# Kernel tuning notes

Hardware: AMD Instinct MI355X
Metric: run time of the kernel (lower is better)

Reference implementation:

```python
import jax, jax.numpy as jnp
import numpy as np

B, S, D, H = 2, 2048, 1024, 16
DK = D // H


def setup_inputs() -> dict:
    key = jax.random.key(0)
    ks = jax.random.split(key, 12)
    scale = 1.0 / np.sqrt(D)
    inp = {
        "q": jax.random.normal(ks[0], (B, S, D), dtype=jnp.float32),
        "k": jax.random.normal(ks[1], (B, S, D), dtype=jnp.float32),
        "v": jax.random.normal(ks[2], (B, S, D), dtype=jnp.float32),
        "mask": jax.random.randint(ks[3], (B, 1, 1, S), 0, 2, dtype=jnp.int32),
        "Wq": jax.random.normal(ks[4], (D, D), dtype=jnp.float32) * scale,
        "bq": jnp.zeros((D,), dtype=jnp.float32),
        "Wk": jax.random.normal(ks[5], (D, D), dtype=jnp.float32) * scale,
        "bk": jnp.zeros((D,), dtype=jnp.float32),
        "Wv": jax.random.normal(ks[6], (D, D), dtype=jnp.float32) * scale,
        "bv": jnp.zeros((D,), dtype=jnp.float32),
        "Wo": jax.random.normal(ks[7], (D, D), dtype=jnp.float32) * scale,
        "bo": jnp.zeros((D,), dtype=jnp.float32),
    }
    return inp


def reference(q, k, v, mask, Wq, bq, Wk, bk, Wv, bv, Wo, bo):
    # Linear projections (torch nn.Linear: x @ W.T + b)
    query = q @ Wq.T + bq                      # [B,S,D]
    key = k @ Wk.T + bk
    value = v @ Wv.T + bv
    # split heads -> [B,H,S,DK]
    def split(x):
        return x.reshape(B, S, H, DK).transpose(0, 2, 1, 3)
    qh, kh, vh = split(query), split(key), split(value)
    # scaled dot-product attention with additive mask
    scores = jnp.einsum("bhqd,bhkd->bhqk", qh, kh) / jnp.sqrt(jnp.float32(DK))
    scores = jnp.where(mask == 0, jnp.float32(-1e9), scores)
    attn = jax.nn.softmax(scores, axis=-1)     # [B,H,S,S]
    out = jnp.einsum("bhqk,bhkd->bhqd", attn, vh)
    out = out.transpose(0, 2, 1, 3).reshape(B, S, D)
    return out @ Wo.T + bo
```

## Files before the change

kernel.cpp:

```cpp
#include <hip/hip_runtime.h>


constexpr int BB = 2;
constexpr int SS = 2048;
constexpr int DD = 1024;
constexpr int HH = 16;
constexpr int DKK = 64;

typedef float f32x4 __attribute__((ext_vector_type(4)));
typedef __bf16 bf16x8 __attribute__((ext_vector_type(8)));
typedef short s16x8 __attribute__((ext_vector_type(8)));
typedef short s16x4 __attribute__((ext_vector_type(4)));

#define DEV static __device__ __forceinline__

DEV f32x4 mfma16(s16x8 a, s16x8 b, f32x4 c) {
  return __builtin_amdgcn_mfma_f32_16x16x32_bf16(
      __builtin_bit_cast(bf16x8, a), __builtin_bit_cast(bf16x8, b), c, 0, 0, 0);
}

DEV void split1(float x, short& h, short& l) {
  unsigned u = __float_as_uint(x);
  h = (short)(u >> 16);
  float hf = __uint_as_float(u & 0xffff0000u);
  l = (short)(__float_as_uint(x - hf) >> 16);
}
DEV short f2bf_rne(float x) {
  unsigned u = __float_as_uint(x);
  return (short)((u + 0x7fffu + ((u >> 16) & 1u)) >> 16);
}
DEV s16x8 load8s(const short* p) { return *(const s16x8*)p; }

DEV void gld_lds16(const short* g, short* l) {
  __builtin_amdgcn_global_load_lds(
      (const __attribute__((address_space(1))) void*)g,
      (__attribute__((address_space(3))) void*)l, 16, 0, 0);
}

__global__ __launch_bounds__(256) void split_pair(const float* __restrict__ X,
                                                  short* __restrict__ H,
                                                  short* __restrict__ L) {
  int i = (blockIdx.x * 256 + threadIdx.x) * 4;
  float4 x = *(const float4*)(X + i);
  float xs[4] = {x.x, x.y, x.z, x.w};
  s16x4 h4, l4;
#pragma unroll
  for (int e = 0; e < 4; ++e) {
    short h, l;
    split1(xs[e], h, l);
    h4[e] = h;
    l4[e] = l;
  }
  *(s16x4*)(H + i) = h4;
  *(s16x4*)(L + i) = l4;
}

__global__ __launch_bounds__(256) void cast_rne(const float* __restrict__ X,
                                                short* __restrict__ Y) {
  int i = (blockIdx.x * 256 + threadIdx.x) * 4;
  float4 x = *(const float4*)(X + i);
  float xs[4] = {x.x, x.y, x.z, x.w};
  s16x4 y4;
#pragma unroll
  for (int e = 0; e < 4; ++e) y4[e] = f2bf_rne(xs[e]);
  *(s16x4*)(Y + i) = y4;
}

template <int SPLIT, int EPI>
__global__ __launch_bounds__(256) void gemm_tile(
    const short* __restrict__ Agh, const short* __restrict__ Agl,
    const short* __restrict__ Wgh, const short* __restrict__ Wgl,
    const float* __restrict__ bias, void* __restrict__ O1, void* __restrict__ O2) {
  __shared__ short lds[2][12288];

  const int tid = threadIdx.x;
  const int lane = tid & 63, wv = tid >> 6;
  const int lo16 = lane & 15, quad = lane >> 4;
  const int m0 = (blockIdx.x & 31) * 128;
  const int n0 = (blockIdx.x >> 5) * 64;

  f32x4 acc[2][4];
#pragma unroll
  for (int mt = 0; mt < 2; ++mt)
#pragma unroll
    for (int nt = 0; nt < 4; ++nt) acc[mt][nt] = f32x4{0.f, 0.f, 0.f, 0.f};

  const int rw = tid >> 2, qw = tid & 3;
  const int ra0 = tid >> 2, ra1 = (tid + 256) >> 2;

  auto stage = [&](int k0, int buf) {
    short* sAh = lds[buf];
    short* sAl = lds[buf] + 4096;
    short* sWh = lds[buf] + 8192;
    short* sWl = lds[buf] + 10240;
    gld_lds16(Wgh + (size_t)(n0 + rw) * DD + k0 + qw * 8, sWh + tid * 8);
    if constexpr (SPLIT)
      gld_lds16(Wgl + (size_t)(n0 + rw) * DD + k0 + qw * 8, sWl + tid * 8);
    gld_lds16(Agh + (size_t)(m0 + ra0) * DD + k0 + qw * 8, sAh + tid * 8);
    gld_lds16(Agh + (size_t)(m0 + ra1) * DD + k0 + qw * 8, sAh + (tid + 256) * 8);
    if constexpr (SPLIT) {
      gld_lds16(Agl + (size_t)(m0 + ra0) * DD + k0 + qw * 8, sAl + tid * 8);
      gld_lds16(Agl + (size_t)(m0 + ra1) * DD + k0 + qw * 8, sAl + (tid + 256) * 8);
    }
  };

  stage(0, 0);

  for (int kk = 0; kk < DD / 32; ++kk) {
    __syncthreads();
    if (kk + 1 < DD / 32) stage((kk + 1) * 32, (kk + 1) & 1);

    const short* sAh = lds[kk & 1];
    const short* sAl = lds[kk & 1] + 4096;
    const short* sWh = lds[kk & 1] + 8192;
    const short* sWl = lds[kk & 1] + 10240;

    s16x8 ah[2], al[2], wh[4], wl[4];
#pragma unroll
    for (int mt = 0; mt < 2; ++mt) {
      const int r = wv * 32 + mt * 16 + lo16;
      ah[mt] = *(const s16x8*)&sAh[r * 32 + quad * 8];
      if constexpr (SPLIT) al[mt] = *(const s16x8*)&sAl[r * 32 + quad * 8];
    }
#pragma unroll
    for (int nt = 0; nt < 4; ++nt) {
      const int r = nt * 16 + lo16;
      wh[nt] = *(const s16x8*)&sWh[r * 32 + quad * 8];
      if constexpr (SPLIT) wl[nt] = *(const s16x8*)&sWl[r * 32 + quad * 8];
    }
#pragma unroll
    for (int mt = 0; mt < 2; ++mt)
#pragma unroll
      for (int nt = 0; nt < 4; ++nt) {
        acc[mt][nt] = mfma16(ah[mt], wh[nt], acc[mt][nt]);
        if constexpr (SPLIT) {
          acc[mt][nt] = mfma16(ah[mt], wl[nt], acc[mt][nt]);
          acc[mt][nt] = mfma16(al[mt], wh[nt], acc[mt][nt]);
        }
      }
  }

#pragma unroll
  for (int mt = 0; mt < 2; ++mt)
#pragma unroll
    for (int nt = 0; nt < 4; ++nt) {
      const int n = n0 + nt * 16 + lo16;
      const float bv = bias[n];
#pragma unroll
      for (int r = 0; r < 4; ++r) {
        const int m = m0 + wv * 32 + mt * 16 + quad * 4 + r;
        const float val = acc[mt][nt][r] + bv;
        const int b = m >> 11, s = m & 2047;
        const int h = n >> 6, dk = n & 63;
        if constexpr (EPI == 0) {
          size_t idx = ((size_t)(b * HH + h) * SS + s) * DKK + dk;
          short hh, ll;
          split1(val, hh, ll);
          ((short*)O1)[idx] = hh;
          ((short*)O2)[idx] = ll;
        } else if constexpr (EPI == 1) {
          size_t idx = ((size_t)(b * HH + h) * DKK + dk) * SS + s;
          ((short*)O1)[idx] = f2bf_rne(val);
        } else {
          ((float*)O1)[(size_t)m * DD + n] = val;
        }
      }
    }
}

constexpr int PAD = 68;
constexpr int NKB = SS / 64;

__global__ __launch_bounds__(256, 2) void mha_attn(
    const short* __restrict__ Qh, const short* __restrict__ Ql,
    const short* __restrict__ Kh, const short* __restrict__ Kl,
    const short* __restrict__ Vt, const int* __restrict__ mask,
    short* __restrict__ Ah, short* __restrict__ Al) {
  __shared__ short sKh[64 * PAD];
  __shared__ short sKl[64 * PAD];
  __shared__ short sV[64 * PAD];
  __shared__ short sP[4][32 * PAD];

  const int tid = threadIdx.x;
  const int lane = tid & 63, wv = tid >> 6;
  const int lo16 = lane & 15, quad = lane >> 4;
  const int bid = blockIdx.x;
  const int head = (bid & 7) * 4 + ((bid >> 3) & 3);
  const int qblk = bid >> 5;
  const int q0 = qblk * 128 + wv * 32;
  const int b = head >> 4;

  const size_t hbase = (size_t)head * SS;

  s16x8 qh[2][2], ql[2][2];
#pragma unroll
  for (int rt = 0; rt < 2; ++rt) {
    size_t qb = (hbase + q0 + rt * 16 + lo16) * DKK + quad * 8;
#pragma unroll
    for (int c = 0; c < 2; ++c) {
      qh[rt][c] = load8s(Qh + qb + c * 32);
      ql[rt][c] = load8s(Ql + qb + c * 32);
    }
  }

  f32x4 Oacc[2][4];
#pragma unroll
  for (int rt = 0; rt < 2; ++rt)
#pragma unroll
    for (int t = 0; t < 4; ++t) Oacc[rt][t] = f32x4{0.f, 0.f, 0.f, 0.f};
  float lsum[2][4];
#pragma unroll
  for (int rt = 0; rt < 2; ++rt)
#pragma unroll
    for (int r = 0; r < 4; ++r) lsum[rt][r] = 0.f;

  const int srow = tid >> 2;
  const int scol0 = (tid & 3) * 8;

  s16x8 rKh[2], rKl[2], rV[2];
#pragma unroll
  for (int i = 0; i < 2; ++i) {
    const int sc_ = scol0 + i * 32;
    rKh[i] = load8s(Kh + (hbase + srow) * DKK + sc_);
    rKl[i] = load8s(Kl + (hbase + srow) * DKK + sc_);
    rV[i] = load8s(Vt + ((size_t)head * DKK + srow) * SS + sc_);
  }

  for (int kb = 0; kb < NKB; ++kb) {
    const int k0g = kb * 64;
#pragma unroll
    for (int i = 0; i < 2; ++i) {
      const int sc_ = scol0 + i * 32;
      *(s16x8*)&sKh[srow * PAD + sc_] = rKh[i];
      *(s16x8*)&sKl[srow * PAD + sc_] = rKl[i];
      *(s16x8*)&sV[srow * PAD + sc_] = rV[i];
    }
    __syncthreads();

    if (kb + 1 < NKB) {
      const int k0n = k0g + 64;
#pragma unroll
      for (int i = 0; i < 2; ++i) {
        const int sc_ = scol0 + i * 32;
        rKh[i] = load8s(Kh + (hbase + k0n + srow) * DKK + sc_);
        rKl[i] = load8s(Kl + (hbase + k0n + srow) * DKK + sc_);
        rV[i] = load8s(Vt + ((size_t)head * DKK + srow) * SS + k0n + sc_);
      }
    }

    f32x4 sc4[2][4];
    int mv[4];
#pragma unroll
    for (int sub = 0; sub < 4; ++sub) {
      mv[sub] = mask[b * SS + k0g + sub * 16 + lo16];
      sc4[0][sub] = f32x4{0.f, 0.f, 0.f, 0.f};
      sc4[1][sub] = f32x4{0.f, 0.f, 0.f, 0.f};
      const int krow = sub * 16 + lo16;
#pragma unroll
      for (int c = 0; c < 2; ++c) {
        s16x8 kh = *(const s16x8*)&sKh[krow * PAD + c * 32 + quad * 8];
        s16x8 kl = *(const s16x8*)&sKl[krow * PAD + c * 32 + quad * 8];
#pragma unroll
        for (int rt = 0; rt < 2; ++rt) {
          sc4[rt][sub] = mfma16(qh[rt][c], kh, sc4[rt][sub]);
          sc4[rt][sub] = mfma16(qh[rt][c], kl, sc4[rt][sub]);
          sc4[rt][sub] = mfma16(ql[rt][c], kh, sc4[rt][sub]);
        }
      }
    }

#pragma unroll
    for (int rt = 0; rt < 2; ++rt)
#pragma unroll
      for (int sub = 0; sub < 4; ++sub)
#pragma unroll
        for (int r = 0; r < 4; ++r) {
          float p = __expf(sc4[rt][sub][r] * 0.125f);
          p = mv[sub] ? p : 0.f;
          lsum[rt][r] += p;
          sP[wv][(rt * 16 + quad * 4 + r) * PAD + sub * 16 + lo16] = f2bf_rne(p);
        }

    s16x8 pa[2][2];
#pragma unroll
    for (int rt = 0; rt < 2; ++rt)
#pragma unroll
      for (int c = 0; c < 2; ++c)
        pa[rt][c] = *(const s16x8*)&sP[wv][(rt * 16 + lo16) * PAD + c * 32 + quad * 8];
#pragma unroll
    for (int t = 0; t < 4; ++t)
#pragma unroll
      for (int c = 0; c < 2; ++c) {
        s16x8 vb = *(const s16x8*)&sV[(t * 16 + lo16) * PAD + c * 32 + quad * 8];
#pragma unroll
        for (int rt = 0; rt < 2; ++rt)
          Oacc[rt][t] = mfma16(pa[rt][c], vb, Oacc[rt][t]);
      }
    __syncthreads();
  }

  const int h = head & 15;
#pragma unroll
  for (int rt = 0; rt < 2; ++rt)
#pragma unroll
    for (int r = 0; r < 4; ++r) {
      float s = lsum[rt][r];
#pragma unroll
      for (int off = 1; off < 16; off <<= 1) s += __shfl_xor(s, off);
      const float rinv = 1.0f / s;
#pragma unroll
      for (int t = 0; t < 4; ++t) {
        const float val = Oacc[rt][t][r] * rinv;
        const int row = q0 + rt * 16 + quad * 4 + r;
        const int col = h * DKK + t * 16 + lo16;
        const size_t idx = ((size_t)b * SS + row) * DD + col;
        short hh, ll;
        split1(val, hh, ll);
        Ah[idx] = hh;
        Al[idx] = ll;
      }
    }
}

extern "C" void kernel_launch(void* const* d_in, const int* in_sizes, int n_in,
                              void* d_out, int out_size, void* d_ws, size_t ws_size,
                              hipStream_t stream) {
  const float* q = (const float*)d_in[0];
  const float* k = (const float*)d_in[1];
  const float* v = (const float*)d_in[2];
  const int* mask = (const int*)d_in[3];
  const float* Wq = (const float*)d_in[4];
  const float* bq = (const float*)d_in[5];
  const float* Wk = (const float*)d_in[6];
  const float* bk = (const float*)d_in[7];
  const float* Wv = (const float*)d_in[8];
  const float* bv = (const float*)d_in[9];
  const float* Wo = (const float*)d_in[10];
  const float* bo = (const float*)d_in[11];

  char* ws = (char*)d_ws;
  size_t off = 0;
  auto take = [&](size_t bytes) {
    char* p = ws + off;
    off += (bytes + 255) & ~(size_t)255;
    return p;
  };
  const size_t WE = (size_t)DD * DD;
  const size_t TE = (size_t)BB * SS * DD;

  short* Wqh = (short*)take(WE * 2);
  short* Wql = (short*)take(WE * 2);
  short* Wkh = (short*)take(WE * 2);
  short* Wkl = (short*)take(WE * 2);
  short* Wvh = (short*)take(WE * 2);
  short* Woh = (short*)take(WE * 2);
  short* Wol = (short*)take(WE * 2);
  short* actH = (short*)take(TE * 2);
  short* actL = (short*)take(TE * 2);
  short* Qh = (short*)take(TE * 2);
  short* Ql = (short*)take(TE * 2);
  short* Kh = (short*)take(TE * 2);
  short* Kl = (short*)take(TE * 2);
  short* Vt = (short*)take(TE * 2);
  (void)ws_size;

  split_pair<<<1024, 256, 0, stream>>>(Wq, Wqh, Wql);
  split_pair<<<1024, 256, 0, stream>>>(Wk, Wkh, Wkl);
  split_pair<<<1024, 256, 0, stream>>>(Wo, Woh, Wol);
  cast_rne<<<1024, 256, 0, stream>>>(Wv, Wvh);

  split_pair<<<4096, 256, 0, stream>>>(q, actH, actL);
  gemm_tile<1, 0><<<512, 256, 0, stream>>>(actH, actL, Wqh, Wql, bq, Qh, Ql);
  split_pair<<<4096, 256, 0, stream>>>(k, actH, actL);
  gemm_tile<1, 0><<<512, 256, 0, stream>>>(actH, actL, Wkh, Wkl, bk, Kh, Kl);
  cast_rne<<<4096, 256, 0, stream>>>(v, actH);
  gemm_tile<0, 1><<<512, 256, 0, stream>>>(actH, nullptr, Wvh, nullptr, bv, Vt, nullptr);

  mha_attn<<<512, 256, 0, stream>>>(Qh, Ql, Kh, Kl, Vt, mask, actH, actL);

  gemm_tile<1, 2><<<512, 256, 0, stream>>>(actH, actL, Woh, Wol, bo, d_out, nullptr);
}
```

Before: 334.4 us.

## Drop Q low-part split and fuse Q/K projection GEMMs into one launch

Q is stored as a single RNE bf16 value, so attention computes scores with two MFMAs (qh*kh, qh*kl) instead of three. This removes a third of the QK matrix work and the Ql loads. The Q and K projection GEMMs are merged into one kernel with 1024 blocks, selected by block index, to fill the GPU better and save a launch. Workspace buffers are reused across stages. The risk is lower accuracy in the scores, since Q keeps only bf16 precision.

```diff
diff --git a/kernel.cpp b/kernel.cpp
--- a/kernel.cpp
+++ b/kernel.cpp
@@ -64,6 +64,111 @@
 #pragma unroll
   for (int e = 0; e < 4; ++e) y4[e] = f2bf_rne(xs[e]);
   *(s16x4*)(Y + i) = y4;
+}
+
+__global__ __launch_bounds__(256) void gemm_qk(
+    const short* __restrict__ qAh, const short* __restrict__ qAl,
+    const short* __restrict__ Wqh, const short* __restrict__ Wql,
+    const float* __restrict__ bq, short* __restrict__ Qo,
+    const short* __restrict__ kAh, const short* __restrict__ kAl,
+    const short* __restrict__ Wkh, const short* __restrict__ Wkl,
+    const float* __restrict__ bk, short* __restrict__ Kho,
+    short* __restrict__ Klo) {
+  __shared__ short lds[2][12288];
+
+  const int tid = threadIdx.x;
+  const int lane = tid & 63, wv = tid >> 6;
+  const int lo16 = lane & 15, quad = lane >> 4;
+  const int sel = blockIdx.x >> 9;
+  const int bid = blockIdx.x & 511;
+  const int m0 = (bid & 31) * 128;
+  const int n0 = (bid >> 5) * 64;
+
+  const short* Agh = sel ? kAh : qAh;
+  const short* Agl = sel ? kAl : qAl;
+  const short* Wgh = sel ? Wkh : Wqh;
+  const short* Wgl = sel ? Wkl : Wql;
+  const float* bias = sel ? bk : bq;
+
+  f32x4 acc[2][4];
+#pragma unroll
+  for (int mt = 0; mt < 2; ++mt)
+#pragma unroll
+    for (int nt = 0; nt < 4; ++nt) acc[mt][nt] = f32x4{0.f, 0.f, 0.f, 0.f};
+
+  const int rw = tid >> 2, qw = tid & 3;
+  const int ra0 = tid >> 2, ra1 = (tid + 256) >> 2;
+
+  auto stage = [&](int k0, int buf) {
+    short* sAh = lds[buf];
+    short* sAl = lds[buf] + 4096;
+    short* sWh = lds[buf] + 8192;
+    short* sWl = lds[buf] + 10240;
+    gld_lds16(Wgh + (size_t)(n0 + rw) * DD + k0 + qw * 8, sWh + tid * 8);
+    gld_lds16(Wgl + (size_t)(n0 + rw) * DD + k0 + qw * 8, sWl + tid * 8);
+    gld_lds16(Agh + (size_t)(m0 + ra0) * DD + k0 + qw * 8, sAh + tid * 8);
+    gld_lds16(Agh + (size_t)(m0 + ra1) * DD + k0 + qw * 8, sAh + (tid + 256) * 8);
+    gld_lds16(Agl + (size_t)(m0 + ra0) * DD + k0 + qw * 8, sAl + tid * 8);
+    gld_lds16(Agl + (size_t)(m0 + ra1) * DD + k0 + qw * 8, sAl + (tid + 256) * 8);
+  };
+
+  stage(0, 0);
+
+  for (int kk = 0; kk < DD / 32; ++kk) {
+    __syncthreads();
+    if (kk + 1 < DD / 32) stage((kk + 1) * 32, (kk + 1) & 1);
+
+    const short* sAh = lds[kk & 1];
+    const short* sAl = lds[kk & 1] + 4096;
+    const short* sWh = lds[kk & 1] + 8192;
+    const short* sWl = lds[kk & 1] + 10240;
+
+    s16x8 ah[2], al[2], wh[4], wl[4];
+#pragma unroll
+    for (int mt = 0; mt < 2; ++mt) {
+      const int r = wv * 32 + mt * 16 + lo16;
+      ah[mt] = *(const s16x8*)&sAh[r * 32 + quad * 8];
+      al[mt] = *(const s16x8*)&sAl[r * 32 + quad * 8];
+    }
+#pragma unroll
+    for (int nt = 0; nt < 4; ++nt) {
+      const int r = nt * 16 + lo16;
+      wh[nt] = *(const s16x8*)&sWh[r * 32 + quad * 8];
+      wl[nt] = *(const s16x8*)&sWl[r * 32 + quad * 8];
+    }
+#pragma unroll
+    for (int mt = 0; mt < 2; ++mt)
+#pragma unroll
+      for (int nt = 0; nt < 4; ++nt) {
+        acc[mt][nt] = mfma16(ah[mt], wh[nt], acc[mt][nt]);
+        acc[mt][nt] = mfma16(ah[mt], wl[nt], acc[mt][nt]);
+        acc[mt][nt] = mfma16(al[mt], wh[nt], acc[mt][nt]);
+      }
+  }
+
+#pragma unroll
+  for (int mt = 0; mt < 2; ++mt)
+#pragma unroll
+    for (int nt = 0; nt < 4; ++nt) {
+      const int n = n0 + nt * 16 + lo16;
+      const float bv = bias[n];
+#pragma unroll
+      for (int r = 0; r < 4; ++r) {
+        const int m = m0 + wv * 32 + mt * 16 + quad * 4 + r;
+        const float val = acc[mt][nt][r] + bv;
+        const int b = m >> 11, s = m & 2047;
+        const int h = n >> 6, dk = n & 63;
+        size_t idx = ((size_t)(b * HH + h) * SS + s) * DKK + dk;
+        if (sel == 0) {
+          Qo[idx] = f2bf_rne(val);
+        } else {
+          short hh, ll;
+          split1(val, hh, ll);
+          Kho[idx] = hh;
+          Klo[idx] = ll;
+        }
+      }
+    }
 }
 
 template <int SPLIT, int EPI>
@@ -152,13 +257,7 @@
         const float val = acc[mt][nt][r] + bv;
         const int b = m >> 11, s = m & 2047;
         const int h = n >> 6, dk = n & 63;
-        if constexpr (EPI == 0) {
-          size_t idx = ((size_t)(b * HH + h) * SS + s) * DKK + dk;
-          short hh, ll;
-          split1(val, hh, ll);
-          ((short*)O1)[idx] = hh;
-          ((short*)O2)[idx] = ll;
-        } else if constexpr (EPI == 1) {
+        if constexpr (EPI == 1) {
           size_t idx = ((size_t)(b * HH + h) * DKK + dk) * SS + s;
           ((short*)O1)[idx] = f2bf_rne(val);
         } else {
@@ -172,10 +271,10 @@
 constexpr int NKB = SS / 64;
 
 __global__ __launch_bounds__(256, 2) void mha_attn(
-    const short* __restrict__ Qh, const short* __restrict__ Ql,
-    const short* __restrict__ Kh, const short* __restrict__ Kl,
-    const short* __restrict__ Vt, const int* __restrict__ mask,
-    short* __restrict__ Ah, short* __restrict__ Al) {
+    const short* __restrict__ Qh, const short* __restrict__ Kh,
+    const short* __restrict__ Kl, const short* __restrict__ Vt,
+    const int* __restrict__ mask, short* __restrict__ Ah,
+    short* __restrict__ Al) {
   __shared__ short sKh[64 * PAD];
   __shared__ short sKl[64 * PAD];
   __shared__ short sV[64 * PAD];
@@ -192,15 +291,12 @@
 
   const size_t hbase = (size_t)head * SS;
 
-  s16x8 qh[2][2], ql[2][2];
+  s16x8 qh[2][2];
 #pragma unroll
   for (int rt = 0; rt < 2; ++rt) {
     size_t qb = (hbase + q0 + rt * 16 + lo16) * DKK + quad * 8;
 #pragma unroll
-    for (int c = 0; c < 2; ++c) {
-      qh[rt][c] = load8s(Qh + qb + c * 32);
-      ql[rt][c] = load8s(Ql + qb + c * 32);
-    }
+    for (int c = 0; c < 2; ++c) qh[rt][c] = load8s(Qh + qb + c * 32);
   }
 
   f32x4 Oacc[2][4];
@@ -264,7 +360,6 @@
         for (int rt = 0; rt < 2; ++rt) {
           sc4[rt][sub] = mfma16(qh[rt][c], kh, sc4[rt][sub]);
           sc4[rt][sub] = mfma16(qh[rt][c], kl, sc4[rt][sub]);
-          sc4[rt][sub] = mfma16(ql[rt][c], kh, sc4[rt][sub]);
         }
       }
     }
@@ -355,28 +450,34 @@
   short* Wvh = (short*)take(WE * 2);
   short* Woh = (short*)take(WE * 2);
   short* Wol = (short*)take(WE * 2);
-  short* actH = (short*)take(TE * 2);
-  short* actL = (short*)take(TE * 2);
+  short* qH = (short*)take(TE * 2);
+  short* qL = (short*)take(TE * 2);
+  short* kH = (short*)take(TE * 2);
+  short* kL = (short*)take(TE * 2);
   short* Qh = (short*)take(TE * 2);
-  short* Ql = (short*)take(TE * 2);
   short* Kh = (short*)take(TE * 2);
   short* Kl = (short*)take(TE * 2);
-  short* Vt = (short*)take(TE * 2);
   (void)ws_size;
+  short* vH = qH;
+  short* Vt = qL;
+  short* aH = kH;
+  short* aL = kL;
 
   split_pair<<<1024, 256, 0, stream>>>(Wq, Wqh, Wql);
   split_pair<<<1024, 256, 0, stream>>>(Wk, Wkh, Wkl);
   split_pair<<<1024, 256, 0, stream>>>(Wo, Woh, Wol);
   cast_rne<<<1024, 256, 0, stream>>>(Wv, Wvh);
 
-  split_pair<<<4096, 256, 0, stream>>>(q, actH, actL);
-  gemm_tile<1, 0><<<512, 256, 0, stream>>>(actH, actL, Wqh, Wql, bq, Qh, Ql);
-  split_pair<<<4096, 256, 0, stream>>>(k, actH, actL);
-  gemm_tile<1, 0><<<512, 256, 0, stream>>>(actH, actL, Wkh, Wkl, bk, Kh, Kl);
-  cast_rne<<<4096, 256, 0, stream>>>(v, actH);
-  gemm_tile<0, 1><<<512, 256, 0, stream>>>(actH, nullptr, Wvh, nullptr, bv, Vt, nullptr);
-
-  mha_attn<<<512, 256, 0, stream>>>(Qh, Ql, Kh, Kl, Vt, mask, actH, actL);
-
-  gemm_tile<1, 2><<<512, 256, 0, stream>>>(actH, actL, Woh, Wol, bo, d_out, nullptr);
-}
+  split_pair<<<4096, 256, 0, stream>>>(q, qH, qL);
+  split_pair<<<4096, 256, 0, stream>>>(k, kH, kL);
+
+  gemm_qk<<<1024, 256, 0, stream>>>(qH, qL, Wqh, Wql, bq, Qh,
+                                    kH, kL, Wkh, Wkl, bk, Kh, Kl);
+
+  cast_rne<<<4096, 256, 0, stream>>>(v, vH);
+  gemm_tile<0, 1><<<512, 256, 0, stream>>>(vH, nullptr, Wvh, nullptr, bv, Vt, nullptr);
+
+  mha_attn<<<512, 256, 0, stream>>>(Qh, Kh, Kl, Vt, mask, aH, aL);
+
+  gemm_tile<1, 2><<<512, 256, 0, stream>>>(aH, aL, Woh, Wol, bo, d_out, nullptr);
+}
```

After: 332.2 us. No clear change (-0.6%).
